# Kernel optimization log

Measured on AMD Instinct MI355X. Metric: run time of the kernel, lower is better.

Reference implementation:

```python
import jax, jax.numpy as jnp
import numpy as np

N_ATOMS = 100000
N_BONDS = 200000
MAX_NB = 6
N_ATOM_FEATS = 39
N_BOND_FEATS = 11
HIDDEN = 128
DEPTH = 6


def setup_inputs() -> dict:
    key = jax.random.key(0)
    k = jax.random.split(key, 8)
    fatoms = jax.random.normal(k[0], (N_ATOMS, N_ATOM_FEATS), dtype=jnp.float32)
    fbonds = jax.random.normal(k[1], (N_BONDS, N_ATOM_FEATS + N_BOND_FEATS), dtype=jnp.float32)
    agraph = jax.random.randint(k[2], (N_ATOMS, MAX_NB), 0, N_BONDS, dtype=jnp.int32)
    bgraph = jax.random.randint(k[3], (N_BONDS, MAX_NB), 0, N_BONDS, dtype=jnp.int32)
    s_i = 1.0 / np.sqrt(N_ATOM_FEATS + N_BOND_FEATS)
    s_h = 1.0 / np.sqrt(HIDDEN)
    s_o = 1.0 / np.sqrt(N_ATOM_FEATS + HIDDEN)
    W_i = jax.random.uniform(k[4], (HIDDEN, N_ATOM_FEATS + N_BOND_FEATS), jnp.float32, -s_i, s_i)
    W_h = jax.random.uniform(k[5], (HIDDEN, HIDDEN), jnp.float32, -s_h, s_h)
    W_o = jax.random.uniform(k[6], (HIDDEN, N_ATOM_FEATS + HIDDEN), jnp.float32, -s_o, s_o)
    b_o = jax.random.uniform(k[7], (HIDDEN,), jnp.float32, -s_o, s_o)
    return {"fatoms": fatoms, "fbonds": fbonds, "agraph": agraph, "bgraph": bgraph,
            "W_i": W_i, "W_h": W_h, "W_o": W_o, "b_o": b_o}


def reference(fatoms, fbonds, agraph, bgraph, W_i, W_h, W_o, b_o):
    # Input message per directed bond: [n_bonds, hidden]
    binput = fbonds @ W_i.T
    message = jax.nn.relu(binput)
    # Message passing: gather neighbor bond messages, sum, linear, residual-add input, ReLU
    for _ in range(DEPTH - 1):
        nei = jnp.take(message, bgraph, axis=0).sum(axis=1)   # [n_bonds, hidden]
        message = jax.nn.relu(binput + nei @ W_h.T)
    # Aggregate incoming bond messages per atom
    a_nei = jnp.take(message, agraph, axis=0).sum(axis=1)      # [n_atoms, hidden]
    atom_input = jnp.concatenate([fatoms, a_nei], axis=1)      # dropout is identity at eval
    atom_h = jax.nn.relu(atom_input @ W_o.T + b_o)
    return atom_h
```

## Files before the change

### kernel.cpp

```cpp
#include <hip/hip_runtime.h>

#define N_ATOMS   100000
#define N_BONDS   200000
#define MAX_NB    6
#define AF        39
#define BFEAT     50
#define H         128
#define DEPTH     6
#define KO        192
#define KS_I      2
#define KS_H      4
#define KS_O      6

typedef unsigned short ushort_t;
typedef unsigned int   uint_t;

typedef __attribute__((ext_vector_type(8))) short  bf16x8;
typedef __attribute__((ext_vector_type(4))) float  f32x4;

__device__ inline float bf2f(ushort_t u) {
    union { uint_t i; float f; } v; v.i = ((uint_t)u) << 16; return v.f;
}
__device__ inline ushort_t f2bf(float f) {
    union { float f; uint_t i; } v; v.f = f;
    uint_t x = v.i;
    uint_t r = (x + 0x7fffu + ((x >> 16) & 1u)) >> 16;
    return (ushort_t)r;
}
__device__ inline uint_t pack2(float a, float b) {
    return (uint_t)f2bf(a) | ((uint_t)f2bf(b) << 16);
}
__device__ inline uint_t relu2(uint_t w) {
    uint_t lo = w & 0xffffu, hi = w >> 16;
    if (lo & 0x8000u) lo = 0;
    if (hi & 0x8000u) hi = 0;
    return lo | (hi << 16);
}
__device__ inline void addv(float* a, uint4 v) {
    a[0] += bf2f((ushort_t)(v.x & 0xffffu)); a[1] += bf2f((ushort_t)(v.x >> 16));
    a[2] += bf2f((ushort_t)(v.y & 0xffffu)); a[3] += bf2f((ushort_t)(v.y >> 16));
    a[4] += bf2f((ushort_t)(v.z & 0xffffu)); a[5] += bf2f((ushort_t)(v.z >> 16));
    a[6] += bf2f((ushort_t)(v.w & 0xffffu)); a[7] += bf2f((ushort_t)(v.w >> 16));
}

__global__ __launch_bounds__(256) void k_pack(const float* __restrict__ W_i,
                                              const float* __restrict__ W_h,
                                              const float* __restrict__ W_o,
                                              ushort_t* __restrict__ pWi,
                                              ushort_t* __restrict__ pWh,
                                              ushort_t* __restrict__ pWo) {
    int id = blockIdx.x * 256 + threadIdx.x;
    int mat;
    ushort_t* dst;
    if (id < 1024)        { mat = 0; dst = pWi; }
    else if (id < 3072)   { mat = 1; dst = pWh; id -= 1024; }
    else                  { mat = 2; dst = pWo; id -= 3072; }
    const int lane = id & 63;
    const int nt   = (id >> 6) & 7;
    const int ks   = id >> 9;
    const int n  = nt * 16 + (lane & 15);
    const int k0 = ks * 32 + (lane >> 4) * 8;
    float v[8];
#pragma unroll
    for (int j = 0; j < 8; ++j) {
        const int k = k0 + j;
        float x = 0.f;
        if (mat == 0)      { if (k < BFEAT) x = W_i[n * BFEAT + k]; }
        else if (mat == 1) { x = W_h[n * H + k]; }
        else {
            if (k < H)          x = W_o[(size_t)n * (AF + H) + AF + k];
            else if (k < H + AF) x = W_o[(size_t)n * (AF + H) + (k - H)];
        }
        v[j] = x;
    }
    uint4 u;
    u.x = pack2(v[0], v[1]); u.y = pack2(v[2], v[3]);
    u.z = pack2(v[4], v[5]); u.w = pack2(v[6], v[7]);
    ((uint4*)dst)[id] = u;
}

__global__ __launch_bounds__(256) void k_binput(const float* __restrict__ fbonds,
                                                const ushort_t* __restrict__ pWi,
                                                ushort_t* __restrict__ binput,
                                                ushort_t* __restrict__ msg) {
    __shared__ __align__(16) ushort_t sAC[64][136];
    const int t = threadIdx.x;
    const int b0 = blockIdx.x * 64;

    for (int i = t; i < 64 * 64; i += 256) {
        const int row = i >> 6, k = i & 63;
        sAC[row][k] = (k < BFEAT) ? f2bf(fbonds[(size_t)(b0 + row) * BFEAT + k]) : (ushort_t)0;
    }
    __syncthreads();

    const int w    = t >> 6;
    const int lane = t & 63;
    const int col  = lane & 15;
    const int kg   = lane >> 4;
    const int m    = 16 * w + col;

    f32x4 acc[8];
#pragma unroll
    for (int nt = 0; nt < 8; ++nt) acc[nt] = (f32x4){0.f, 0.f, 0.f, 0.f};
    bf16x8 af[KS_I];
#pragma unroll
    for (int ks = 0; ks < KS_I; ++ks)
        af[ks] = *(const bf16x8*)&sAC[m][ks * 32 + kg * 8];
#pragma unroll
    for (int ks = 0; ks < KS_I; ++ks) {
#pragma unroll
        for (int nt = 0; nt < 8; ++nt) {
            const bf16x8 b = *(const bf16x8*)(pWi + (((size_t)(ks * 8 + nt) * 64 + lane) * 8));
            acc[nt] = __builtin_amdgcn_mfma_f32_16x16x32_bf16(af[ks], b, acc[nt], 0, 0, 0);
        }
    }
    const int row0 = kg * 4;
#pragma unroll
    for (int nt = 0; nt < 8; ++nt)
#pragma unroll
        for (int r = 0; r < 4; ++r)
            sAC[16 * w + row0 + r][nt * 16 + col] = f2bf(acc[nt][r]);
    __syncthreads();

    for (int i = t; i < 64 * 16; i += 256) {
        const int row = i >> 4, c0 = (i & 15) * 8;
        const uint4 v = *(const uint4*)&sAC[row][c0];
        uint4 rl;
        rl.x = relu2(v.x); rl.y = relu2(v.y); rl.z = relu2(v.z); rl.w = relu2(v.w);
        const size_t off = (size_t)(b0 + row) * H + c0;
        *(uint4*)(binput + off) = v;
        *(uint4*)(msg + off)    = rl;
    }
}

__global__ __launch_bounds__(256) void k_mp(const ushort_t* __restrict__ msg_in,
                                            const int* __restrict__ bgraph,
                                            const ushort_t* __restrict__ pWh,
                                            const ushort_t* __restrict__ binput,
                                            ushort_t* __restrict__ msg_out) {
    __shared__ __align__(16) ushort_t sAC[64][136];
    __shared__ int sIdx[64][MAX_NB];
    const int t = threadIdx.x;
    const int b0 = blockIdx.x * 64;

    for (int i = t; i < 64 * MAX_NB; i += 256)
        sIdx[i / MAX_NB][i % MAX_NB] = bgraph[(size_t)b0 * MAX_NB + i];
    __syncthreads();

    {
        const int bi = t >> 4;
        const int c0 = (t & 15) * 8;
#pragma unroll
        for (int p = 0; p < 4; ++p) {
            const int i = p * 16 + bi;
            const int* ip = sIdx[i];
            const int j0 = ip[0], j1 = ip[1], j2 = ip[2], j3 = ip[3], j4 = ip[4], j5 = ip[5];
            const uint4 v0 = *(const uint4*)(msg_in + (size_t)j0 * H + c0);
            const uint4 v1 = *(const uint4*)(msg_in + (size_t)j1 * H + c0);
            const uint4 v2 = *(const uint4*)(msg_in + (size_t)j2 * H + c0);
            const uint4 v3 = *(const uint4*)(msg_in + (size_t)j3 * H + c0);
            const uint4 v4 = *(const uint4*)(msg_in + (size_t)j4 * H + c0);
            const uint4 v5 = *(const uint4*)(msg_in + (size_t)j5 * H + c0);
            float a[8];
#pragma unroll
            for (int q = 0; q < 8; ++q) a[q] = 0.f;
            addv(a, v0); addv(a, v1); addv(a, v2); addv(a, v3); addv(a, v4); addv(a, v5);
            uint4 u;
            u.x = pack2(a[0], a[1]); u.y = pack2(a[2], a[3]);
            u.z = pack2(a[4], a[5]); u.w = pack2(a[6], a[7]);
            *(uint4*)&sAC[i][c0] = u;
        }
    }
    __syncthreads();

    const int w    = t >> 6;
    const int lane = t & 63;
    const int col  = lane & 15;
    const int kg   = lane >> 4;
    const int m    = 16 * w + col;

    f32x4 acc[8];
#pragma unroll
    for (int nt = 0; nt < 8; ++nt) acc[nt] = (f32x4){0.f, 0.f, 0.f, 0.f};
    bf16x8 af[KS_H];
#pragma unroll
    for (int ks = 0; ks < KS_H; ++ks)
        af[ks] = *(const bf16x8*)&sAC[m][ks * 32 + kg * 8];
#pragma unroll
    for (int ks = 0; ks < KS_H; ++ks) {
#pragma unroll
        for (int nt = 0; nt < 8; ++nt) {
            const bf16x8 b = *(const bf16x8*)(pWh + (((size_t)(ks * 8 + nt) * 64 + lane) * 8));
            acc[nt] = __builtin_amdgcn_mfma_f32_16x16x32_bf16(af[ks], b, acc[nt], 0, 0, 0);
        }
    }
    const int row0 = kg * 4;
#pragma unroll
    for (int nt = 0; nt < 8; ++nt)
#pragma unroll
        for (int r = 0; r < 4; ++r)
            sAC[16 * w + row0 + r][nt * 16 + col] = f2bf(acc[nt][r]);
    __syncthreads();

    for (int i = t; i < 64 * 16; i += 256) {
        const int row = i >> 4, c0 = (i & 15) * 8;
        const size_t off = (size_t)(b0 + row) * H + c0;
        const uint4 bi4 = *(const uint4*)(binput + off);
        const uint4 cc  = *(const uint4*)&sAC[row][c0];
        uint4 o; float v0, v1;
        v0 = bf2f((ushort_t)(bi4.x & 0xffffu)) + bf2f((ushort_t)(cc.x & 0xffffu));
        v1 = bf2f((ushort_t)(bi4.x >> 16))     + bf2f((ushort_t)(cc.x >> 16));
        o.x = pack2(v0 > 0.f ? v0 : 0.f, v1 > 0.f ? v1 : 0.f);
        v0 = bf2f((ushort_t)(bi4.y & 0xffffu)) + bf2f((ushort_t)(cc.y & 0xffffu));
        v1 = bf2f((ushort_t)(bi4.y >> 16))     + bf2f((ushort_t)(cc.y >> 16));
        o.y = pack2(v0 > 0.f ? v0 : 0.f, v1 > 0.f ? v1 : 0.f);
        v0 = bf2f((ushort_t)(bi4.z & 0xffffu)) + bf2f((ushort_t)(cc.z & 0xffffu));
        v1 = bf2f((ushort_t)(bi4.z >> 16))     + bf2f((ushort_t)(cc.z >> 16));
        o.z = pack2(v0 > 0.f ? v0 : 0.f, v1 > 0.f ? v1 : 0.f);
        v0 = bf2f((ushort_t)(bi4.w & 0xffffu)) + bf2f((ushort_t)(cc.w & 0xffffu));
        v1 = bf2f((ushort_t)(bi4.w >> 16))     + bf2f((ushort_t)(cc.w >> 16));
        o.w = pack2(v0 > 0.f ? v0 : 0.f, v1 > 0.f ? v1 : 0.f);
        *(uint4*)(msg_out + off) = o;
    }
}

__global__ __launch_bounds__(256) void k_out(const ushort_t* __restrict__ msg,
                                             const int* __restrict__ agraph,
                                             const float* __restrict__ fatoms,
                                             const ushort_t* __restrict__ pWo,
                                             const float* __restrict__ b_o,
                                             float* __restrict__ out) {
    __shared__ __align__(16) unsigned char smem[64 * 132 * 4];
    ushort_t (*sA)[200] = (ushort_t(*)[200])smem;
    float    (*sC)[132] = (float(*)[132])smem;
    __shared__ int sIdx[64][MAX_NB];
    const int t = threadIdx.x;
    const int a0 = blockIdx.x * 64;

    for (int i = t; i < 64 * MAX_NB; i += 256) {
        const int a = a0 + i / MAX_NB;
        sIdx[i / MAX_NB][i % MAX_NB] = (a < N_ATOMS) ? agraph[(size_t)a * MAX_NB + (i % MAX_NB)] : 0;
    }
    for (int i = t; i < 64 * 64; i += 256) {
        const int row = i >> 6, c = i & 63;
        const int a = a0 + row;
        float x = 0.f;
        if (c < AF && a < N_ATOMS) x = fatoms[(size_t)a * AF + c];
        sA[row][H + c] = f2bf(x);
    }
    __syncthreads();

    {
        const int bi = t >> 4;
        const int c0 = (t & 15) * 8;
#pragma unroll
        for (int p = 0; p < 4; ++p) {
            const int i = p * 16 + bi;
            const int* ip = sIdx[i];
            const int j0 = ip[0], j1 = ip[1], j2 = ip[2], j3 = ip[3], j4 = ip[4], j5 = ip[5];
            const uint4 v0 = *(const uint4*)(msg + (size_t)j0 * H + c0);
            const uint4 v1 = *(const uint4*)(msg + (size_t)j1 * H + c0);
            const uint4 v2 = *(const uint4*)(msg + (size_t)j2 * H + c0);
            const uint4 v3 = *(const uint4*)(msg + (size_t)j3 * H + c0);
            const uint4 v4 = *(const uint4*)(msg + (size_t)j4 * H + c0);
            const uint4 v5 = *(const uint4*)(msg + (size_t)j5 * H + c0);
            float a[8];
#pragma unroll
            for (int q = 0; q < 8; ++q) a[q] = 0.f;
            addv(a, v0); addv(a, v1); addv(a, v2); addv(a, v3); addv(a, v4); addv(a, v5);
            uint4 u;
            u.x = pack2(a[0], a[1]); u.y = pack2(a[2], a[3]);
            u.z = pack2(a[4], a[5]); u.w = pack2(a[6], a[7]);
            *(uint4*)&sA[i][c0] = u;
        }
    }
    __syncthreads();

    const int w    = t >> 6;
    const int lane = t & 63;
    const int col  = lane & 15;
    const int kg   = lane >> 4;
    const int m    = 16 * w + col;

    f32x4 acc[8];
#pragma unroll
    for (int nt = 0; nt < 8; ++nt) acc[nt] = (f32x4){0.f, 0.f, 0.f, 0.f};
#pragma unroll
    for (int ks = 0; ks < KS_O; ++ks) {
        const bf16x8 a = *(const bf16x8*)&sA[m][ks * 32 + kg * 8];
#pragma unroll
        for (int nt = 0; nt < 8; ++nt) {
            const bf16x8 b = *(const bf16x8*)(pWo + (((size_t)(ks * 8 + nt) * 64 + lane) * 8));
            acc[nt] = __builtin_amdgcn_mfma_f32_16x16x32_bf16(a, b, acc[nt], 0, 0, 0);
        }
    }
    __syncthreads();

    const int row0 = kg * 4;
#pragma unroll
    for (int nt = 0; nt < 8; ++nt)
#pragma unroll
        for (int r = 0; r < 4; ++r)
            sC[16 * w + row0 + r][nt * 16 + col] = acc[nt][r];
    __syncthreads();

    const float4* bo4 = (const float4*)b_o;
    for (int i = t; i < 64 * 16; i += 256) {
        const int row = i >> 4, c0 = (i & 15) * 8;
        const int a = a0 + row;
        if (a < N_ATOMS) {
            const float* cp = &sC[row][c0];
            const float4 b1 = bo4[c0 >> 2];
            const float4 b2 = bo4[(c0 >> 2) + 1];
            float4 o1, o2;
            o1.x = cp[0] + b1.x; o1.y = cp[1] + b1.y; o1.z = cp[2] + b1.z; o1.w = cp[3] + b1.w;
            o2.x = cp[4] + b2.x; o2.y = cp[5] + b2.y; o2.z = cp[6] + b2.z; o2.w = cp[7] + b2.w;
            o1.x = o1.x > 0.f ? o1.x : 0.f; o1.y = o1.y > 0.f ? o1.y : 0.f;
            o1.z = o1.z > 0.f ? o1.z : 0.f; o1.w = o1.w > 0.f ? o1.w : 0.f;
            o2.x = o2.x > 0.f ? o2.x : 0.f; o2.y = o2.y > 0.f ? o2.y : 0.f;
            o2.z = o2.z > 0.f ? o2.z : 0.f; o2.w = o2.w > 0.f ? o2.w : 0.f;
            float* op = out + (size_t)a * H + c0;
            *(float4*)op = o1;
            *(float4*)(op + 4) = o2;
        }
    }
}

extern "C" void kernel_launch(void* const* d_in, const int* in_sizes, int n_in,
                              void* d_out, int out_size, void* d_ws, size_t ws_size,
                              hipStream_t stream) {
    const float* fatoms = (const float*)d_in[0];
    const float* fbonds = (const float*)d_in[1];
    const int*   agraph = (const int*)d_in[2];
    const int*   bgraph = (const int*)d_in[3];
    const float* W_i    = (const float*)d_in[4];
    const float* W_h    = (const float*)d_in[5];
    const float* W_o    = (const float*)d_in[6];
    const float* b_o    = (const float*)d_in[7];
    float* out = (float*)d_out;

    const size_t MSG_BYTES = (size_t)N_BONDS * H * sizeof(ushort_t);
    char* ws = (char*)d_ws;
    ushort_t* binput = (ushort_t*)(ws);
    ushort_t* msgA   = (ushort_t*)(ws + MSG_BYTES);
    ushort_t* msgB   = (ushort_t*)(ws + 2 * MSG_BYTES);
    ushort_t* pWi    = (ushort_t*)(ws + 3 * MSG_BYTES);
    ushort_t* pWh    = (ushort_t*)(ws + 3 * MSG_BYTES + 16 * 1024);
    ushort_t* pWo    = (ushort_t*)(ws + 3 * MSG_BYTES + 48 * 1024);

    k_pack<<<24, 256, 0, stream>>>(W_i, W_h, W_o, pWi, pWh, pWo);
    k_binput<<<N_BONDS / 64, 256, 0, stream>>>(fbonds, pWi, binput, msgA);

    ushort_t* cur = msgA;
    ushort_t* nxt = msgB;
    for (int d = 0; d < DEPTH - 1; ++d) {
        k_mp<<<N_BONDS / 64, 256, 0, stream>>>(cur, bgraph, pWh, binput, nxt);
        ushort_t* tmp = cur; cur = nxt; nxt = tmp;
    }

    k_out<<<(N_ATOMS + 63) / 64, 256, 0, stream>>>(cur, agraph, fatoms, pWo, b_o, out);
}
```

Before: 527.8 us.

## Gather neighbor sums directly into MFMA A-fragments, drop block-wide barriers

The message-passing and output kernels now have each lane gather and sum its own row's neighbor messages straight into its MFMA A-operand registers. This replaces staging the summed rows through shared memory behind __syncthreads. The epilogue uses a per-wave shared tile guarded only by an lgkmcnt wait rather than block barriers, and the output kernel builds its fatoms fragments in registers too. Gather access changes from 16 lanes covering one full row to each lane taking 16-byte pieces from different rows. That reduces coalescing per instruction and raises register pressure.

Measured after the change: 544.4 us. 3.1% more time.

```diff
diff --git a/kernel.cpp b/kernel.cpp
--- a/kernel.cpp
+++ b/kernel.cpp
@@ -7,7 +7,6 @@
 #define BFEAT     50
 #define H         128
 #define DEPTH     6
-#define KO        192
 #define KS_I      2
 #define KS_H      4
 #define KS_O      6
@@ -41,6 +40,12 @@
     a[2] += bf2f((ushort_t)(v.y & 0xffffu)); a[3] += bf2f((ushort_t)(v.y >> 16));
     a[4] += bf2f((ushort_t)(v.z & 0xffffu)); a[5] += bf2f((ushort_t)(v.z >> 16));
     a[6] += bf2f((ushort_t)(v.w & 0xffffu)); a[7] += bf2f((ushort_t)(v.w >> 16));
+}
+__device__ inline bf16x8 pack8(const float* a) {
+    union { uint4 u; bf16x8 h; } c;
+    c.u.x = pack2(a[0], a[1]); c.u.y = pack2(a[2], a[3]);
+    c.u.z = pack2(a[4], a[5]); c.u.w = pack2(a[6], a[7]);
+    return c.h;
 }
 
 __global__ __launch_bounds__(256) void k_pack(const float* __restrict__ W_i,
@@ -138,54 +143,38 @@
                                             const ushort_t* __restrict__ pWh,
                                             const ushort_t* __restrict__ binput,
                                             ushort_t* __restrict__ msg_out) {
-    __shared__ __align__(16) ushort_t sAC[64][136];
-    __shared__ int sIdx[64][MAX_NB];
+    __shared__ __align__(16) ushort_t sC[4][16][136];
     const int t = threadIdx.x;
-    const int b0 = blockIdx.x * 64;
-
-    for (int i = t; i < 64 * MAX_NB; i += 256)
-        sIdx[i / MAX_NB][i % MAX_NB] = bgraph[(size_t)b0 * MAX_NB + i];
-    __syncthreads();
-
-    {
-        const int bi = t >> 4;
-        const int c0 = (t & 15) * 8;
-#pragma unroll
-        for (int p = 0; p < 4; ++p) {
-            const int i = p * 16 + bi;
-            const int* ip = sIdx[i];
-            const int j0 = ip[0], j1 = ip[1], j2 = ip[2], j3 = ip[3], j4 = ip[4], j5 = ip[5];
-            const uint4 v0 = *(const uint4*)(msg_in + (size_t)j0 * H + c0);
-            const uint4 v1 = *(const uint4*)(msg_in + (size_t)j1 * H + c0);
-            const uint4 v2 = *(const uint4*)(msg_in + (size_t)j2 * H + c0);
-            const uint4 v3 = *(const uint4*)(msg_in + (size_t)j3 * H + c0);
-            const uint4 v4 = *(const uint4*)(msg_in + (size_t)j4 * H + c0);
-            const uint4 v5 = *(const uint4*)(msg_in + (size_t)j5 * H + c0);
-            float a[8];
-#pragma unroll
-            for (int q = 0; q < 8; ++q) a[q] = 0.f;
-            addv(a, v0); addv(a, v1); addv(a, v2); addv(a, v3); addv(a, v4); addv(a, v5);
-            uint4 u;
-            u.x = pack2(a[0], a[1]); u.y = pack2(a[2], a[3]);
-            u.z = pack2(a[4], a[5]); u.w = pack2(a[6], a[7]);
-            *(uint4*)&sAC[i][c0] = u;
-        }
-    }
-    __syncthreads();
-
     const int w    = t >> 6;
     const int lane = t & 63;
-    const int col  = lane & 15;
-    const int kg   = lane >> 4;
-    const int m    = 16 * w + col;
+    const int r    = lane & 15;
+    const int cg   = lane >> 4;
+    const int rowg = blockIdx.x * 64 + w * 16 + r;
+
+    const int* ip = bgraph + (size_t)rowg * MAX_NB;
+    int idx[MAX_NB];
+#pragma unroll
+    for (int j = 0; j < MAX_NB; ++j) idx[j] = ip[j];
+
+    bf16x8 af[KS_H];
+#pragma unroll
+    for (int ks = 0; ks < KS_H; ++ks) {
+        const int c0 = ks * 32 + cg * 8;
+        uint4 v[MAX_NB];
+#pragma unroll
+        for (int j = 0; j < MAX_NB; ++j)
+            v[j] = *(const uint4*)(msg_in + (size_t)idx[j] * H + c0);
+        float a[8];
+#pragma unroll
+        for (int q = 0; q < 8; ++q) a[q] = 0.f;
+#pragma unroll
+        for (int j = 0; j < MAX_NB; ++j) addv(a, v[j]);
+        af[ks] = pack8(a);
+    }
 
     f32x4 acc[8];
 #pragma unroll
     for (int nt = 0; nt < 8; ++nt) acc[nt] = (f32x4){0.f, 0.f, 0.f, 0.f};
-    bf16x8 af[KS_H];
-#pragma unroll
-    for (int ks = 0; ks < KS_H; ++ks)
-        af[ks] = *(const bf16x8*)&sAC[m][ks * 32 + kg * 8];
 #pragma unroll
     for (int ks = 0; ks < KS_H; ++ks) {
 #pragma unroll
@@ -194,19 +183,21 @@
             acc[nt] = __builtin_amdgcn_mfma_f32_16x16x32_bf16(af[ks], b, acc[nt], 0, 0, 0);
         }
     }
-    const int row0 = kg * 4;
+
 #pragma unroll
     for (int nt = 0; nt < 8; ++nt)
 #pragma unroll
-        for (int r = 0; r < 4; ++r)
-            sAC[16 * w + row0 + r][nt * 16 + col] = f2bf(acc[nt][r]);
-    __syncthreads();
-
-    for (int i = t; i < 64 * 16; i += 256) {
-        const int row = i >> 4, c0 = (i & 15) * 8;
-        const size_t off = (size_t)(b0 + row) * H + c0;
+        for (int rr = 0; rr < 4; ++rr)
+            sC[w][cg * 4 + rr][nt * 16 + r] = f2bf(acc[nt][rr]);
+    asm volatile("s_waitcnt lgkmcnt(0)" ::: "memory");
+
+    const int base = blockIdx.x * 64 + w * 16;
+#pragma unroll
+    for (int p = 0; p < 4; ++p) {
+        const int erow = p * 4 + cg;
+        const size_t off = (size_t)(base + erow) * H + r * 8;
+        const uint4 cc  = *(const uint4*)&sC[w][erow][r * 8];
         const uint4 bi4 = *(const uint4*)(binput + off);
-        const uint4 cc  = *(const uint4*)&sAC[row][c0];
         uint4 o; float v0, v1;
         v0 = bf2f((ushort_t)(bi4.x & 0xffffu)) + bf2f((ushort_t)(cc.x & 0xffffu));
         v1 = bf2f((ushort_t)(bi4.x >> 16))     + bf2f((ushort_t)(cc.x >> 16));
@@ -230,88 +221,75 @@
                                              const ushort_t* __restrict__ pWo,
                                              const float* __restrict__ b_o,
                                              float* __restrict__ out) {
-    __shared__ __align__(16) unsigned char smem[64 * 132 * 4];
-    ushort_t (*sA)[200] = (ushort_t(*)[200])smem;
-    float    (*sC)[132] = (float(*)[132])smem;
-    __shared__ int sIdx[64][MAX_NB];
+    __shared__ __align__(16) float sC[4][16][132];
     const int t = threadIdx.x;
-    const int a0 = blockIdx.x * 64;
-
-    for (int i = t; i < 64 * MAX_NB; i += 256) {
-        const int a = a0 + i / MAX_NB;
-        sIdx[i / MAX_NB][i % MAX_NB] = (a < N_ATOMS) ? agraph[(size_t)a * MAX_NB + (i % MAX_NB)] : 0;
-    }
-    for (int i = t; i < 64 * 64; i += 256) {
-        const int row = i >> 6, c = i & 63;
-        const int a = a0 + row;
-        float x = 0.f;
-        if (c < AF && a < N_ATOMS) x = fatoms[(size_t)a * AF + c];
-        sA[row][H + c] = f2bf(x);
-    }
-    __syncthreads();
-
-    {
-        const int bi = t >> 4;
-        const int c0 = (t & 15) * 8;
-#pragma unroll
-        for (int p = 0; p < 4; ++p) {
-            const int i = p * 16 + bi;
-            const int* ip = sIdx[i];
-            const int j0 = ip[0], j1 = ip[1], j2 = ip[2], j3 = ip[3], j4 = ip[4], j5 = ip[5];
-            const uint4 v0 = *(const uint4*)(msg + (size_t)j0 * H + c0);
-            const uint4 v1 = *(const uint4*)(msg + (size_t)j1 * H + c0);
-            const uint4 v2 = *(const uint4*)(msg + (size_t)j2 * H + c0);
-            const uint4 v3 = *(const uint4*)(msg + (size_t)j3 * H + c0);
-            const uint4 v4 = *(const uint4*)(msg + (size_t)j4 * H + c0);
-            const uint4 v5 = *(const uint4*)(msg + (size_t)j5 * H + c0);
-            float a[8];
-#pragma unroll
-            for (int q = 0; q < 8; ++q) a[q] = 0.f;
-            addv(a, v0); addv(a, v1); addv(a, v2); addv(a, v3); addv(a, v4); addv(a, v5);
-            uint4 u;
-            u.x = pack2(a[0], a[1]); u.y = pack2(a[2], a[3]);
-            u.z = pack2(a[4], a[5]); u.w = pack2(a[6], a[7]);
-            *(uint4*)&sA[i][c0] = u;
-        }
-    }
-    __syncthreads();
-
     const int w    = t >> 6;
     const int lane = t & 63;
-    const int col  = lane & 15;
-    const int kg   = lane >> 4;
-    const int m    = 16 * w + col;
+    const int r    = lane & 15;
+    const int cg   = lane >> 4;
+    const int rowg = blockIdx.x * 64 + w * 16 + r;
+    const int rowc = rowg < N_ATOMS ? rowg : N_ATOMS - 1;
+
+    const int* ip = agraph + (size_t)rowc * MAX_NB;
+    int idx[MAX_NB];
+#pragma unroll
+    for (int j = 0; j < MAX_NB; ++j) idx[j] = ip[j];
+
+    bf16x8 af[KS_O];
+#pragma unroll
+    for (int ks = 0; ks < 4; ++ks) {
+        const int c0 = ks * 32 + cg * 8;
+        uint4 v[MAX_NB];
+#pragma unroll
+        for (int j = 0; j < MAX_NB; ++j)
+            v[j] = *(const uint4*)(msg + (size_t)idx[j] * H + c0);
+        float a[8];
+#pragma unroll
+        for (int q = 0; q < 8; ++q) a[q] = 0.f;
+#pragma unroll
+        for (int j = 0; j < MAX_NB; ++j) addv(a, v[j]);
+        af[ks] = pack8(a);
+    }
+#pragma unroll
+    for (int ks = 4; ks < 6; ++ks) {
+        float a[8];
+#pragma unroll
+        for (int q = 0; q < 8; ++q) {
+            const int f = (ks - 4) * 32 + cg * 8 + q;
+            a[q] = (f < AF) ? fatoms[(size_t)rowc * AF + f] : 0.f;
+        }
+        af[ks] = pack8(a);
+    }
 
     f32x4 acc[8];
 #pragma unroll
     for (int nt = 0; nt < 8; ++nt) acc[nt] = (f32x4){0.f, 0.f, 0.f, 0.f};
 #pragma unroll
     for (int ks = 0; ks < KS_O; ++ks) {
-        const bf16x8 a = *(const bf16x8*)&sA[m][ks * 32 + kg * 8];
 #pragma unroll
         for (int nt = 0; nt < 8; ++nt) {
             const bf16x8 b = *(const bf16x8*)(pWo + (((size_t)(ks * 8 + nt) * 64 + lane) * 8));
-            acc[nt] = __builtin_amdgcn_mfma_f32_16x16x32_bf16(a, b, acc[nt], 0, 0, 0);
-        }
-    }
-    __syncthreads();
-
-    const int row0 = kg * 4;
+            acc[nt] = __builtin_amdgcn_mfma_f32_16x16x32_bf16(af[ks], b, acc[nt], 0, 0, 0);
+        }
+    }
+
 #pragma unroll
     for (int nt = 0; nt < 8; ++nt)
 #pragma unroll
-        for (int r = 0; r < 4; ++r)
-            sC[16 * w + row0 + r][nt * 16 + col] = acc[nt][r];
-    __syncthreads();
-
+        for (int rr = 0; rr < 4; ++rr)
+            sC[w][cg * 4 + rr][nt * 16 + r] = acc[nt][rr];
+    asm volatile("s_waitcnt lgkmcnt(0)" ::: "memory");
+
+    const int base = blockIdx.x * 64 + w * 16;
     const float4* bo4 = (const float4*)b_o;
-    for (int i = t; i < 64 * 16; i += 256) {
-        const int row = i >> 4, c0 = (i & 15) * 8;
-        const int a = a0 + row;
+#pragma unroll
+    for (int p = 0; p < 4; ++p) {
+        const int erow = p * 4 + cg;
+        const int a = base + erow;
         if (a < N_ATOMS) {
-            const float* cp = &sC[row][c0];
-            const float4 b1 = bo4[c0 >> 2];
-            const float4 b2 = bo4[(c0 >> 2) + 1];
+            const float* cp = &sC[w][erow][r * 8];
+            const float4 b1 = bo4[r * 2];
+            const float4 b2 = bo4[r * 2 + 1];
             float4 o1, o2;
             o1.x = cp[0] + b1.x; o1.y = cp[1] + b1.y; o1.z = cp[2] + b1.z; o1.w = cp[3] + b1.w;
             o2.x = cp[4] + b2.x; o2.y = cp[5] + b2.y; o2.z = cp[6] + b2.z; o2.w = cp[7] + b2.w;
@@ -319,7 +297,7 @@
             o1.z = o1.z > 0.f ? o1.z : 0.f; o1.w = o1.w > 0.f ? o1.w : 0.f;
             o2.x = o2.x > 0.f ? o2.x : 0.f; o2.y = o2.y > 0.f ? o2.y : 0.f;
             o2.z = o2.z > 0.f ? o2.z : 0.f; o2.w = o2.w > 0.f ? o2.w : 0.f;
-            float* op = out + (size_t)a * H + c0;
+            float* op = out + (size_t)a * H + r * 8;
             *(float4*)op = o1;
             *(float4*)(op + 4) = o2;
         }
```

## Defer ReLU into gather, drop initial message write, batch gathers and prefetch binput

Applied to the files above, without the earlier changes.

Messages are now stored pre-activation and the ReLU is applied when neighbours are gathered, so the binput buffer itself serves as the first message and k_binput no longer writes a separate message array. Gathers for two bonds are issued together to raise memory-level parallelism, and binput rows are prefetched into registers before the MFMA phase. The fbonds load is vectorized to float2. This adds ReLU work per gathered element (six times per output) and more registers in exchange for less memory traffic and better latency hiding.

New measurement: 516.5 us. 1.02x faster.

```diff
diff --git a/kernel.cpp b/kernel.cpp
--- a/kernel.cpp
+++ b/kernel.cpp
@@ -7,7 +7,6 @@
 #define BFEAT     50
 #define H         128
 #define DEPTH     6
-#define KO        192
 #define KS_I      2
 #define KS_H      4
 #define KS_O      6
@@ -41,6 +40,10 @@
     a[2] += bf2f((ushort_t)(v.y & 0xffffu)); a[3] += bf2f((ushort_t)(v.y >> 16));
     a[4] += bf2f((ushort_t)(v.z & 0xffffu)); a[5] += bf2f((ushort_t)(v.z >> 16));
     a[6] += bf2f((ushort_t)(v.w & 0xffffu)); a[7] += bf2f((ushort_t)(v.w >> 16));
+}
+__device__ inline void addvr(float* a, uint4 v) {
+    v.x = relu2(v.x); v.y = relu2(v.y); v.z = relu2(v.z); v.w = relu2(v.w);
+    addv(a, v);
 }
 
 __global__ __launch_bounds__(256) void k_pack(const float* __restrict__ W_i,
@@ -81,15 +84,19 @@
 
 __global__ __launch_bounds__(256) void k_binput(const float* __restrict__ fbonds,
                                                 const ushort_t* __restrict__ pWi,
-                                                ushort_t* __restrict__ binput,
-                                                ushort_t* __restrict__ msg) {
+                                                ushort_t* __restrict__ binput) {
     __shared__ __align__(16) ushort_t sAC[64][136];
     const int t = threadIdx.x;
     const int b0 = blockIdx.x * 64;
 
-    for (int i = t; i < 64 * 64; i += 256) {
-        const int row = i >> 6, k = i & 63;
-        sAC[row][k] = (k < BFEAT) ? f2bf(fbonds[(size_t)(b0 + row) * BFEAT + k]) : (ushort_t)0;
+    for (int i = t; i < 64 * 25; i += 256) {
+        const int row = i / 25, j = i % 25;
+        const float2 v = *(const float2*)(fbonds + (size_t)(b0 + row) * BFEAT + j * 2);
+        *(uint_t*)&sAC[row][j * 2] = pack2(v.x, v.y);
+    }
+    for (int i = t; i < 64 * 7; i += 256) {
+        const int row = i / 7, c = BFEAT + (i % 7) * 2;
+        *(uint_t*)&sAC[row][c] = 0u;
     }
     __syncthreads();
 
@@ -125,11 +132,7 @@
     for (int i = t; i < 64 * 16; i += 256) {
         const int row = i >> 4, c0 = (i & 15) * 8;
         const uint4 v = *(const uint4*)&sAC[row][c0];
-        uint4 rl;
-        rl.x = relu2(v.x); rl.y = relu2(v.y); rl.z = relu2(v.z); rl.w = relu2(v.w);
-        const size_t off = (size_t)(b0 + row) * H + c0;
-        *(uint4*)(binput + off) = v;
-        *(uint4*)(msg + off)    = rl;
+        *(uint4*)(binput + (size_t)(b0 + row) * H + c0) = v;
     }
 }
 
@@ -151,27 +154,41 @@
         const int bi = t >> 4;
         const int c0 = (t & 15) * 8;
 #pragma unroll
-        for (int p = 0; p < 4; ++p) {
-            const int i = p * 16 + bi;
-            const int* ip = sIdx[i];
-            const int j0 = ip[0], j1 = ip[1], j2 = ip[2], j3 = ip[3], j4 = ip[4], j5 = ip[5];
-            const uint4 v0 = *(const uint4*)(msg_in + (size_t)j0 * H + c0);
-            const uint4 v1 = *(const uint4*)(msg_in + (size_t)j1 * H + c0);
-            const uint4 v2 = *(const uint4*)(msg_in + (size_t)j2 * H + c0);
-            const uint4 v3 = *(const uint4*)(msg_in + (size_t)j3 * H + c0);
-            const uint4 v4 = *(const uint4*)(msg_in + (size_t)j4 * H + c0);
-            const uint4 v5 = *(const uint4*)(msg_in + (size_t)j5 * H + c0);
-            float a[8];
-#pragma unroll
-            for (int q = 0; q < 8; ++q) a[q] = 0.f;
-            addv(a, v0); addv(a, v1); addv(a, v2); addv(a, v3); addv(a, v4); addv(a, v5);
-            uint4 u;
-            u.x = pack2(a[0], a[1]); u.y = pack2(a[2], a[3]);
-            u.z = pack2(a[4], a[5]); u.w = pack2(a[6], a[7]);
-            *(uint4*)&sAC[i][c0] = u;
-        }
-    }
-    __syncthreads();
+        for (int p = 0; p < 4; p += 2) {
+            const int iA = p * 16 + bi;
+            const int iB = iA + 16;
+            uint4 vA[MAX_NB], vB[MAX_NB];
+#pragma unroll
+            for (int j = 0; j < MAX_NB; ++j)
+                vA[j] = *(const uint4*)(msg_in + (size_t)sIdx[iA][j] * H + c0);
+#pragma unroll
+            for (int j = 0; j < MAX_NB; ++j)
+                vB[j] = *(const uint4*)(msg_in + (size_t)sIdx[iB][j] * H + c0);
+            float a[8], b[8];
+#pragma unroll
+            for (int q = 0; q < 8; ++q) { a[q] = 0.f; b[q] = 0.f; }
+#pragma unroll
+            for (int j = 0; j < MAX_NB; ++j) addvr(a, vA[j]);
+#pragma unroll
+            for (int j = 0; j < MAX_NB; ++j) addvr(b, vB[j]);
+            uint4 ua, ub;
+            ua.x = pack2(a[0], a[1]); ua.y = pack2(a[2], a[3]);
+            ua.z = pack2(a[4], a[5]); ua.w = pack2(a[6], a[7]);
+            ub.x = pack2(b[0], b[1]); ub.y = pack2(b[2], b[3]);
+            ub.z = pack2(b[4], b[5]); ub.w = pack2(b[6], b[7]);
+            *(uint4*)&sAC[iA][c0] = ua;
+            *(uint4*)&sAC[iB][c0] = ub;
+        }
+    }
+    __syncthreads();
+
+    uint4 biPF[4];
+#pragma unroll
+    for (int p = 0; p < 4; ++p) {
+        const int i = t + p * 256;
+        const int row = i >> 4, c0 = (i & 15) * 8;
+        biPF[p] = *(const uint4*)(binput + (size_t)(b0 + row) * H + c0);
+    }
 
     const int w    = t >> 6;
     const int lane = t & 63;
@@ -202,24 +219,26 @@
             sAC[16 * w + row0 + r][nt * 16 + col] = f2bf(acc[nt][r]);
     __syncthreads();
 
-    for (int i = t; i < 64 * 16; i += 256) {
+#pragma unroll
+    for (int p = 0; p < 4; ++p) {
+        const int i = t + p * 256;
         const int row = i >> 4, c0 = (i & 15) * 8;
         const size_t off = (size_t)(b0 + row) * H + c0;
-        const uint4 bi4 = *(const uint4*)(binput + off);
+        const uint4 bi4 = biPF[p];
         const uint4 cc  = *(const uint4*)&sAC[row][c0];
         uint4 o; float v0, v1;
         v0 = bf2f((ushort_t)(bi4.x & 0xffffu)) + bf2f((ushort_t)(cc.x & 0xffffu));
         v1 = bf2f((ushort_t)(bi4.x >> 16))     + bf2f((ushort_t)(cc.x >> 16));
-        o.x = pack2(v0 > 0.f ? v0 : 0.f, v1 > 0.f ? v1 : 0.f);
+        o.x = pack2(v0, v1);
         v0 = bf2f((ushort_t)(bi4.y & 0xffffu)) + bf2f((ushort_t)(cc.y & 0xffffu));
         v1 = bf2f((ushort_t)(bi4.y >> 16))     + bf2f((ushort_t)(cc.y >> 16));
-        o.y = pack2(v0 > 0.f ? v0 : 0.f, v1 > 0.f ? v1 : 0.f);
+        o.y = pack2(v0, v1);
         v0 = bf2f((ushort_t)(bi4.z & 0xffffu)) + bf2f((ushort_t)(cc.z & 0xffffu));
         v1 = bf2f((ushort_t)(bi4.z >> 16))     + bf2f((ushort_t)(cc.z >> 16));
-        o.z = pack2(v0 > 0.f ? v0 : 0.f, v1 > 0.f ? v1 : 0.f);
+        o.z = pack2(v0, v1);
         v0 = bf2f((ushort_t)(bi4.w & 0xffffu)) + bf2f((ushort_t)(cc.w & 0xffffu));
         v1 = bf2f((ushort_t)(bi4.w >> 16))     + bf2f((ushort_t)(cc.w >> 16));
-        o.w = pack2(v0 > 0.f ? v0 : 0.f, v1 > 0.f ? v1 : 0.f);
+        o.w = pack2(v0, v1);
         *(uint4*)(msg_out + off) = o;
     }
 }
@@ -254,24 +273,30 @@
         const int bi = t >> 4;
         const int c0 = (t & 15) * 8;
 #pragma unroll
-        for (int p = 0; p < 4; ++p) {
-            const int i = p * 16 + bi;
-            const int* ip = sIdx[i];
-            const int j0 = ip[0], j1 = ip[1], j2 = ip[2], j3 = ip[3], j4 = ip[4], j5 = ip[5];
-            const uint4 v0 = *(const uint4*)(msg + (size_t)j0 * H + c0);
-            const uint4 v1 = *(const uint4*)(msg + (size_t)j1 * H + c0);
-            const uint4 v2 = *(const uint4*)(msg + (size_t)j2 * H + c0);
-            const uint4 v3 = *(const uint4*)(msg + (size_t)j3 * H + c0);
-            const uint4 v4 = *(const uint4*)(msg + (size_t)j4 * H + c0);
-            const uint4 v5 = *(const uint4*)(msg + (size_t)j5 * H + c0);
-            float a[8];
-#pragma unroll
-            for (int q = 0; q < 8; ++q) a[q] = 0.f;
-            addv(a, v0); addv(a, v1); addv(a, v2); addv(a, v3); addv(a, v4); addv(a, v5);
-            uint4 u;
-            u.x = pack2(a[0], a[1]); u.y = pack2(a[2], a[3]);
-            u.z = pack2(a[4], a[5]); u.w = pack2(a[6], a[7]);
-            *(uint4*)&sA[i][c0] = u;
+        for (int p = 0; p < 4; p += 2) {
+            const int iA = p * 16 + bi;
+            const int iB = iA + 16;
+            uint4 vA[MAX_NB], vB[MAX_NB];
+#pragma unroll
+            for (int j = 0; j < MAX_NB; ++j)
+                vA[j] = *(const uint4*)(msg + (size_t)sIdx[iA][j] * H + c0);
+#pragma unroll
+            for (int j = 0; j < MAX_NB; ++j)
+                vB[j] = *(const uint4*)(msg + (size_t)sIdx[iB][j] * H + c0);
+            float a[8], b[8];
+#pragma unroll
+            for (int q = 0; q < 8; ++q) { a[q] = 0.f; b[q] = 0.f; }
+#pragma unroll
+            for (int j = 0; j < MAX_NB; ++j) addvr(a, vA[j]);
+#pragma unroll
+            for (int j = 0; j < MAX_NB; ++j) addvr(b, vB[j]);
+            uint4 ua, ub;
+            ua.x = pack2(a[0], a[1]); ua.y = pack2(a[2], a[3]);
+            ua.z = pack2(a[4], a[5]); ua.w = pack2(a[6], a[7]);
+            ub.x = pack2(b[0], b[1]); ub.y = pack2(b[2], b[3]);
+            ub.z = pack2(b[4], b[5]); ub.w = pack2(b[6], b[7]);
+            *(uint4*)&sA[iA][c0] = ua;
+            *(uint4*)&sA[iB][c0] = ub;
         }
     }
     __syncthreads();
@@ -349,13 +374,14 @@
     ushort_t* pWo    = (ushort_t*)(ws + 3 * MSG_BYTES + 48 * 1024);
 
     k_pack<<<24, 256, 0, stream>>>(W_i, W_h, W_o, pWi, pWh, pWo);
-    k_binput<<<N_BONDS / 64, 256, 0, stream>>>(fbonds, pWi, binput, msgA);
-
-    ushort_t* cur = msgA;
-    ushort_t* nxt = msgB;
+    k_binput<<<N_BONDS / 64, 256, 0, stream>>>(fbonds, pWi, binput);
+
+    ushort_t* bufs[2] = { msgA, msgB };
+    const ushort_t* cur = binput;
     for (int d = 0; d < DEPTH - 1; ++d) {
+        ushort_t* nxt = bufs[d & 1];
         k_mp<<<N_BONDS / 64, 256, 0, stream>>>(cur, bgraph, pWh, binput, nxt);
-        ushort_t* tmp = cur; cur = nxt; nxt = tmp;
+        cur = nxt;
     }
 
     k_out<<<(N_ATOMS + 63) / 64, 256, 0, stream>>>(cur, agraph, fatoms, pWo, b_o, out);
```
